# Kernel tuning notes

Measured on AMD Instinct MI355X. Metric: run time of the kernel, lower is better.

## Reference

```python
import jax, jax.numpy as jnp
import numpy as np

B, L, D = 1, 256, 256
H, DK, R = 8, 32, 2
EPS = 1e-6


def _proj_ode(x, t, W, b, r):
    """Stand-in for ODELinear/InterpLinear: linear projection of x broadcast
    over a second time index with r exponential time-decay coefficients.
    x: [B,L,D], t: [B,L] -> [B,L,L,r,D_out]"""
    base = x @ W.T + b                                  # [B,L,Do]
    dt = jnp.abs(t[:, :, None] - t[:, None, :])         # [B,L,L]
    steps = jnp.linspace(0.0, 1.0, r, dtype=x.dtype)    # [r]
    coef = jnp.exp(-dt[:, :, :, None] * steps)          # [B,L,L,r]
    return coef[..., None] * base[:, None, :, None, :]  # [B,L,L,r,Do]


def _layer_norm(x, g, b):
    mu = x.mean(-1, keepdims=True)
    var = ((x - mu) ** 2).mean(-1, keepdims=True)
    return (x - mu) * jax.lax.rsqrt(var + EPS) * g + b


def setup_inputs() -> dict:
    key = jax.random.key(0)
    ks = jax.random.split(key, 12)
    s = 1.0 / np.sqrt(D)
    return {
        "q": jax.random.normal(ks[0], (B, L, D), jnp.float32),
        "k": jax.random.normal(ks[1], (B, L, D), jnp.float32),
        "v": jax.random.normal(ks[2], (B, L, D), jnp.float32),
        "t": jax.random.uniform(ks[3], (B, L), jnp.float32),
        "Wq": jax.random.normal(ks[4], (D, D), jnp.float32) * s,
        "bq": jnp.zeros((D,), jnp.float32),
        "Wk": jax.random.normal(ks[5], (D, D), jnp.float32) * s,
        "bk": jnp.zeros((D,), jnp.float32),
        "Wv": jax.random.normal(ks[6], (D, D), jnp.float32) * s,
        "bv": jnp.zeros((D,), jnp.float32),
        "fc_w": jax.random.normal(ks[7], (D, D), jnp.float32) * s,
        "fc_b": jnp.zeros((D,), jnp.float32),
        "ln_g": jnp.ones((D,), jnp.float32),
        "ln_b": jnp.zeros((D,), jnp.float32),
    }


def reference(q, k, v, t, Wq, bq, Wk, bk, Wv, bv, fc_w, fc_b, ln_g, ln_b):
    temp = DK ** 0.5
    residual = q
    qn = _layer_norm(q, ln_g, ln_b)  # normalize_before=True (only q)

    # [B,L,L,R,D] -> [B,L,L,R,H,DK] -> [B,H,L,L,R,DK]
    def to6(x):
        return x.reshape(B, L, L, R, H, DK).transpose(0, 4, 1, 2, 3, 5)

    qp = to6(_proj_ode(qn, t, Wq, bq, R))
    kp = to6(_proj_ode(k, t, Wk, bk, R))
    vp = to6(_proj_ode(v, t, Wv, bv, R))

    # attn = (q/temp * k).sum(-1).sum(-1): multiply-reduce over (R, DK), no matmul
    attn = jnp.einsum('bhijrd,bhijrd->bhij', qp, kp) / temp
    attn = jax.nn.softmax(attn, axis=-1)  # dropout=0 (eval)

    vs = vp.sum(axis=4)                                   # reduce R: [B,H,L,L,DK]
    out = jnp.einsum('bhij,bhijd->bhid', attn, vs)        # reduce second L
    out = out.transpose(0, 2, 1, 3).reshape(B, L, H * DK)
    out = out @ fc_w.T + fc_b
    out = out + residual
    return (out, attn)
```

## Files before the change

kernel.cpp:

```cpp
#include <hip/hip_runtime.h>
#include <math.h>


#define INV_TEMP 0.17677669529663687f

__device__ __forceinline__ void gemm_panel(
    const float* __restrict__ X, const float* __restrict__ W,
    const float* __restrict__ bias, const float* __restrict__ res,
    const float* __restrict__ ln_g, const float* __restrict__ ln_b,
    float* __restrict__ out, const int mode) {
  __shared__ float As[256][33];
  __shared__ float Bs[256][33];
  const int t = threadIdx.x;
  const int j0 = blockIdx.y << 5, o0 = blockIdx.x << 5;
  const int lr = t >> 3;
  const int cg = (t & 7) << 2;
  float4 xa[8], wb[8];
#pragma unroll
  for (int u = 0; u < 8; ++u) {
    xa[u] = *(const float4*)(X + ((j0 + lr) << 8) + (u << 5) + cg);
    wb[u] = *(const float4*)(W + ((o0 + lr) << 8) + (u << 5) + cg);
  }
  if (mode == 0) {
    float s = 0.f, s2 = 0.f;
#pragma unroll
    for (int u = 0; u < 8; ++u) {
      s  += xa[u].x + xa[u].y + xa[u].z + xa[u].w;
      s2 += xa[u].x * xa[u].x + xa[u].y * xa[u].y +
            xa[u].z * xa[u].z + xa[u].w * xa[u].w;
    }
#pragma unroll
    for (int off = 1; off < 8; off <<= 1) {
      s  += __shfl_xor(s, off);
      s2 += __shfl_xor(s2, off);
    }
    const float mu = s * 0.00390625f;
    const float rs = rsqrtf(s2 * 0.00390625f - mu * mu + 1e-6f);
#pragma unroll
    for (int u = 0; u < 8; ++u) {
      const float4 gv = *(const float4*)(ln_g + (u << 5) + cg);
      const float4 bv = *(const float4*)(ln_b + (u << 5) + cg);
      xa[u].x = (xa[u].x - mu) * rs * gv.x + bv.x;
      xa[u].y = (xa[u].y - mu) * rs * gv.y + bv.y;
      xa[u].z = (xa[u].z - mu) * rs * gv.z + bv.z;
      xa[u].w = (xa[u].w - mu) * rs * gv.w + bv.w;
    }
  }
#pragma unroll
  for (int u = 0; u < 8; ++u) {
    const int c = (u << 5) + cg;
    As[c + 0][lr] = xa[u].x; As[c + 1][lr] = xa[u].y;
    As[c + 2][lr] = xa[u].z; As[c + 3][lr] = xa[u].w;
    Bs[c + 0][lr] = wb[u].x; Bs[c + 1][lr] = wb[u].y;
    Bs[c + 2][lr] = wb[u].z; Bs[c + 3][lr] = wb[u].w;
  }
  __syncthreads();
  const int tx = t & 15, ty = t >> 4;
  float acc00 = 0.f, acc01 = 0.f, acc10 = 0.f, acc11 = 0.f;
#pragma unroll 16
  for (int kk = 0; kk < 256; ++kk) {
    const float2 av = *(const float2*)&As[kk][ty << 1];
    const float2 bv = *(const float2*)&Bs[kk][tx << 1];
    acc00 = fmaf(av.x, bv.x, acc00);
    acc01 = fmaf(av.x, bv.y, acc01);
    acc10 = fmaf(av.y, bv.x, acc10);
    acc11 = fmaf(av.y, bv.y, acc11);
  }
  const int j = j0 + (ty << 1), o = o0 + (tx << 1);
  const float b0 = bias[o], b1 = bias[o + 1];
  acc00 += b0; acc01 += b1; acc10 += b0; acc11 += b1;
  if (mode <= 1) {
    *(float2*)(out + (o << 8) + j)       = make_float2(acc00, acc10);
    *(float2*)(out + ((o + 1) << 8) + j) = make_float2(acc01, acc11);
  } else {
    float2 r0 = make_float2(0.f, 0.f), r1 = make_float2(0.f, 0.f);
    if (mode == 3) {
      r0 = *(const float2*)(res + (j << 8) + o);
      r1 = *(const float2*)(res + ((j + 1) << 8) + o);
    }
    *(float2*)(out + (j << 8) + o) = make_float2(acc00 + r0.x, acc01 + r0.y);
    *(float2*)(out + ((j + 1) << 8) + o) =
        make_float2(acc10 + r1.x, acc11 + r1.y);
  }
}

__global__ __launch_bounds__(256) void mha_proj_gemm3(
    const float* __restrict__ q, const float* __restrict__ kin,
    const float* __restrict__ vin, const float* __restrict__ Wq,
    const float* __restrict__ bq, const float* __restrict__ Wk,
    const float* __restrict__ bk, const float* __restrict__ Wv,
    const float* __restrict__ bv, const float* __restrict__ ln_g,
    const float* __restrict__ ln_b, float* __restrict__ baseQT,
    float* __restrict__ baseKT, float* __restrict__ baseV) {
  const int z = blockIdx.z;
  if (z == 0)
    gemm_panel(q, Wq, bq, nullptr, ln_g, ln_b, baseQT, 0);
  else if (z == 1)
    gemm_panel(kin, Wk, bk, nullptr, nullptr, nullptr, baseKT, 1);
  else
    gemm_panel(vin, Wv, bv, nullptr, nullptr, nullptr, baseV, 2);
}

__global__ __launch_bounds__(256) void mha_fc_gemm(
    const float* __restrict__ ctxf, const float* __restrict__ fc_w,
    const float* __restrict__ fc_b, const float* __restrict__ q,
    float* __restrict__ out) {
  gemm_panel(ctxf, fc_w, fc_b, q, nullptr, nullptr, out, 3);
}

__global__ __launch_bounds__(512) void mha_attn_fused(
    const float* __restrict__ baseQT, const float* __restrict__ baseKT,
    const float* __restrict__ baseV, const float* __restrict__ tt,
    float* __restrict__ attn_out, float* __restrict__ ctxf) {
  const int h = blockIdx.y;
  const int i0 = blockIdx.x << 3;
  const int t = threadIdx.x;
  __shared__ float s_lds[256];
  __shared__ float P[8][256];
  if (t < 256) {
    const float* qc = baseQT + (h << 13) + t;
    const float* kc = baseKT + (h << 13) + t;
    float acc = 0.f;
#pragma unroll
    for (int dk = 0; dk < 32; ++dk)
      acc = fmaf(qc[dk << 8], kc[dk << 8], acc);
    s_lds[t] = acc * INV_TEMP;
  }
  __syncthreads();

  const int w = t >> 6, lane = t & 63;
  const int i = i0 + w;
  const float ti = tt[i];
  const float4 tj = ((const float4*)tt)[lane];
  const float4 sv = ((const float4*)s_lds)[lane];
  const float e0 = __expf(-fabsf(ti - tj.x));
  const float e1 = __expf(-fabsf(ti - tj.y));
  const float e2 = __expf(-fabsf(ti - tj.z));
  const float e3 = __expf(-fabsf(ti - tj.w));
  const float sc0 = (1.f + e0 * e0) * sv.x;
  const float sc1 = (1.f + e1 * e1) * sv.y;
  const float sc2 = (1.f + e2 * e2) * sv.z;
  const float sc3 = (1.f + e3 * e3) * sv.w;
  float m = fmaxf(fmaxf(sc0, sc1), fmaxf(sc2, sc3));
#pragma unroll
  for (int off = 32; off; off >>= 1) m = fmaxf(m, __shfl_xor(m, off));
  float p0 = __expf(sc0 - m), p1 = __expf(sc1 - m);
  float p2 = __expf(sc2 - m), p3 = __expf(sc3 - m);
  float s = p0 + p1 + p2 + p3;
#pragma unroll
  for (int off = 32; off; off >>= 1) s += __shfl_xor(s, off);
  const float rinv = 1.f / s;
  p0 *= rinv; p1 *= rinv; p2 *= rinv; p3 *= rinv;
  ((float4*)(attn_out + (((h << 8) + i) << 8)))[lane] =
      make_float4(p0, p1, p2, p3);
  ((float4*)P[w])[lane] = make_float4(p0 * (1.f + e0), p1 * (1.f + e1),
                                      p2 * (1.f + e2), p3 * (1.f + e3));

  const int dk = lane & 31, half = lane >> 5;
  const float* Pr = P[w] + (half << 7);
  const float* Vp = baseV + (h << 5) + dk + (half << 15);
  float a0 = 0.f, a1 = 0.f, a2 = 0.f, a3 = 0.f;
#pragma unroll 4
  for (int jj = 0; jj < 128; jj += 4) {
    a0 = fmaf(Pr[jj + 0], Vp[(jj + 0) << 8], a0);
    a1 = fmaf(Pr[jj + 1], Vp[(jj + 1) << 8], a1);
    a2 = fmaf(Pr[jj + 2], Vp[(jj + 2) << 8], a2);
    a3 = fmaf(Pr[jj + 3], Vp[(jj + 3) << 8], a3);
  }
  float acc = (a0 + a1) + (a2 + a3);
  acc += __shfl_xor(acc, 32);
  if (half == 0) ctxf[(i << 8) + (h << 5) + dk] = acc;
}

extern "C" void kernel_launch(void* const* d_in, const int* in_sizes, int n_in,
                              void* d_out, int out_size, void* d_ws,
                              size_t ws_size, hipStream_t stream) {
  const float* q    = (const float*)d_in[0];
  const float* kin  = (const float*)d_in[1];
  const float* vin  = (const float*)d_in[2];
  const float* tt   = (const float*)d_in[3];
  const float* Wq   = (const float*)d_in[4];
  const float* bq   = (const float*)d_in[5];
  const float* Wk   = (const float*)d_in[6];
  const float* bk   = (const float*)d_in[7];
  const float* Wv   = (const float*)d_in[8];
  const float* bv   = (const float*)d_in[9];
  const float* fc_w = (const float*)d_in[10];
  const float* fc_b = (const float*)d_in[11];
  const float* ln_g = (const float*)d_in[12];
  const float* ln_b = (const float*)d_in[13];

  float* out  = (float*)d_out;
  float* attn = out + 65536;

  float* ws     = (float*)d_ws;
  float* baseQT = ws;
  float* baseKT = ws + 65536;
  float* baseV  = ws + 131072;
  float* ctxf   = ws + 196608;

  hipLaunchKernelGGL(mha_proj_gemm3, dim3(8, 8, 3), dim3(256), 0, stream, q,
                     kin, vin, Wq, bq, Wk, bk, Wv, bv, ln_g, ln_b, baseQT,
                     baseKT, baseV);
  hipLaunchKernelGGL(mha_attn_fused, dim3(32, 8), dim3(512), 0, stream,
                     baseQT, baseKT, baseV, tt, attn, ctxf);
  hipLaunchKernelGGL(mha_fc_gemm, dim3(8, 8), dim3(256), 0, stream, ctxf,
                     fc_w, fc_b, q, out);
}
```

Measured before the change: 100.4 us.

## Split GEMM panel K dimension across wavefronts with 4x4 register tiles

Replaces the 2x2-per-thread GEMM inner loop with a split-K scheme. Each of the 4 wavefronts computes a 4x4 register tile over a quarter of K using float4 LDS reads, then the partial sums are combined through an extra shared-memory reduction buffer. The goal is fewer LDS loads per FMA and a shorter serial loop. In exchange it adds a second barrier, more LDS usage (padding changes to 36), and scalar transposed stores for modes 0 and 1.

```diff
diff --git a/kernel.cpp b/kernel.cpp
--- a/kernel.cpp
+++ b/kernel.cpp
@@ -9,8 +9,9 @@
     const float* __restrict__ bias, const float* __restrict__ res,
     const float* __restrict__ ln_g, const float* __restrict__ ln_b,
     float* __restrict__ out, const int mode) {
-  __shared__ float As[256][33];
-  __shared__ float Bs[256][33];
+  __shared__ float As[256][36];
+  __shared__ float Bs[256][36];
+  __shared__ float Red[4][32][36];
   const int t = threadIdx.x;
   const int j0 = blockIdx.y << 5, o0 = blockIdx.x << 5;
   const int lr = t >> 3;
@@ -55,32 +56,62 @@
     Bs[c + 2][lr] = wb[u].z; Bs[c + 3][lr] = wb[u].w;
   }
   __syncthreads();
-  const int tx = t & 15, ty = t >> 4;
-  float acc00 = 0.f, acc01 = 0.f, acc10 = 0.f, acc11 = 0.f;
-#pragma unroll 16
-  for (int kk = 0; kk < 256; ++kk) {
-    const float2 av = *(const float2*)&As[kk][ty << 1];
-    const float2 bv = *(const float2*)&Bs[kk][tx << 1];
-    acc00 = fmaf(av.x, bv.x, acc00);
-    acc01 = fmaf(av.x, bv.y, acc01);
-    acc10 = fmaf(av.y, bv.x, acc10);
-    acc11 = fmaf(av.y, bv.y, acc11);
-  }
-  const int j = j0 + (ty << 1), o = o0 + (tx << 1);
-  const float b0 = bias[o], b1 = bias[o + 1];
-  acc00 += b0; acc01 += b1; acc10 += b0; acc11 += b1;
+
+  const int w = t >> 6, lane = t & 63;
+  const int jb = (lane >> 3) << 2;
+  const int ob = (lane & 7) << 2;
+  const int kbase = w << 6;
+  float acc[4][4] = {{0.f}};
+#pragma unroll 8
+  for (int kk = 0; kk < 64; ++kk) {
+    const float4 av = *(const float4*)&As[kbase + kk][jb];
+    const float4 bv = *(const float4*)&Bs[kbase + kk][ob];
+    acc[0][0] = fmaf(av.x, bv.x, acc[0][0]);
+    acc[0][1] = fmaf(av.x, bv.y, acc[0][1]);
+    acc[0][2] = fmaf(av.x, bv.z, acc[0][2]);
+    acc[0][3] = fmaf(av.x, bv.w, acc[0][3]);
+    acc[1][0] = fmaf(av.y, bv.x, acc[1][0]);
+    acc[1][1] = fmaf(av.y, bv.y, acc[1][1]);
+    acc[1][2] = fmaf(av.y, bv.z, acc[1][2]);
+    acc[1][3] = fmaf(av.y, bv.w, acc[1][3]);
+    acc[2][0] = fmaf(av.z, bv.x, acc[2][0]);
+    acc[2][1] = fmaf(av.z, bv.y, acc[2][1]);
+    acc[2][2] = fmaf(av.z, bv.z, acc[2][2]);
+    acc[2][3] = fmaf(av.z, bv.w, acc[2][3]);
+    acc[3][0] = fmaf(av.w, bv.x, acc[3][0]);
+    acc[3][1] = fmaf(av.w, bv.y, acc[3][1]);
+    acc[3][2] = fmaf(av.w, bv.z, acc[3][2]);
+    acc[3][3] = fmaf(av.w, bv.w, acc[3][3]);
+  }
+#pragma unroll
+  for (int r = 0; r < 4; ++r)
+    *(float4*)&Red[w][jb + r][ob] =
+        make_float4(acc[r][0], acc[r][1], acc[r][2], acc[r][3]);
+  __syncthreads();
+
+  const int j = t >> 3, o4 = (t & 7) << 2;
+  const float4 s0 = *(const float4*)&Red[0][j][o4];
+  const float4 s1 = *(const float4*)&Red[1][j][o4];
+  const float4 s2 = *(const float4*)&Red[2][j][o4];
+  const float4 s3 = *(const float4*)&Red[3][j][o4];
+  const float4 bv4 = *(const float4*)(bias + o0 + o4);
+  float4 rs4;
+  rs4.x = (s0.x + s1.x) + (s2.x + s3.x) + bv4.x;
+  rs4.y = (s0.y + s1.y) + (s2.y + s3.y) + bv4.y;
+  rs4.z = (s0.z + s1.z) + (s2.z + s3.z) + bv4.z;
+  rs4.w = (s0.w + s1.w) + (s2.w + s3.w) + bv4.w;
+  const int gj = j0 + j, go = o0 + o4;
   if (mode <= 1) {
-    *(float2*)(out + (o << 8) + j)       = make_float2(acc00, acc10);
-    *(float2*)(out + ((o + 1) << 8) + j) = make_float2(acc01, acc11);
+    out[((go + 0) << 8) + gj] = rs4.x;
+    out[((go + 1) << 8) + gj] = rs4.y;
+    out[((go + 2) << 8) + gj] = rs4.z;
+    out[((go + 3) << 8) + gj] = rs4.w;
   } else {
-    float2 r0 = make_float2(0.f, 0.f), r1 = make_float2(0.f, 0.f);
     if (mode == 3) {
-      r0 = *(const float2*)(res + (j << 8) + o);
-      r1 = *(const float2*)(res + ((j + 1) << 8) + o);
-    }
-    *(float2*)(out + (j << 8) + o) = make_float2(acc00 + r0.x, acc01 + r0.y);
-    *(float2*)(out + ((j + 1) << 8) + o) =
-        make_float2(acc10 + r1.x, acc11 + r1.y);
+      const float4 rv = *(const float4*)(res + (gj << 8) + go);
+      rs4.x += rv.x; rs4.y += rv.y; rs4.z += rv.z; rs4.w += rv.w;
+    }
+    *(float4*)(out + (gj << 8) + go) = rs4;
   }
 }
 
```

After: 96.54 us. -3.9%, faster.
